# Kernel tuning notes

Hardware: AMD Instinct MI355X
Metric: run time of the kernel (lower is better)

Reference implementation:

```python
import jax, jax.numpy as jnp
import numpy as np

B, S, D = 2, 1024, 512
E, K = 8, 2          # num_experts, top_k (hardcoded in EncoderLayerMOE)
HMOE = 4             # SMoE_MHA heads
HD = D // HMOE       # 128 head dim for local experts
HID = 4 * D          # 2048 expert hidden (both extractors)
AH = 4               # attention heads
DK = D // AH
NEG = -1e9


def layer_norm(x, w, b, eps=1e-12):
    mu = x.mean(-1, keepdims=True)
    var = ((x - mu) ** 2).mean(-1, keepdims=True)
    return (x - mu) * jax.lax.rsqrt(var + eps) * w + b


def moe(x, gate_w, gate_b, w1, b1, w2, b2):
    """Dense all-expert SMoE, gather top-k, re-softmax topk weights (faithful).
    x: [..., d]; w1: [E,d,H]; w2: [E,H,d]."""
    gate_scores = x @ gate_w + gate_b                      # [..., E]
    sm = jax.nn.softmax(gate_scores, axis=-1)
    topk_s, topk_i = jax.lax.top_k(sm, K)                  # [..., K]
    h1 = jax.nn.relu(jnp.einsum('...d,edh->...eh', x, w1) + b1)   # [..., E, H]
    out = jnp.einsum('...eh,ehd->...ed', h1, w2) + b2      # [..., E, d]
    idx = jnp.broadcast_to(topk_i[..., None], topk_i.shape + (out.shape[-1],))
    sel = jnp.take_along_axis(out, idx, axis=-2)           # [..., K, d]
    w = jax.nn.softmax(topk_s, axis=-1)[..., None]         # re-softmax of topk scores
    return (sel * w).sum(-2)


def local_extractor(x, pre_w, pre_b, gate_w, gate_b, w1, b1, w2, b2, align_w, align_b):
    b, s, d = x.shape
    xp = x @ pre_w + pre_b
    xf = xp.reshape(b, s, HMOE, HD).transpose(0, 2, 1, 3)  # [b,h,s,hd]
    eo = moe(xf, gate_w, gate_b, w1, b1, w2, b2)
    xf = xf + eo
    xo = xf.transpose(0, 2, 1, 3).reshape(b, s, d)
    return xo @ align_w + align_b


def mha(xq, xkv, mask, wq, bq, wk, bk, wv, bv, wo, bo):
    b, sq, d = xq.shape
    sk = xkv.shape[1]
    q = (xq @ wq + bq).reshape(b, sq, AH, DK).transpose(0, 2, 1, 3)
    k = (xkv @ wk + bk).reshape(b, sk, AH, DK).transpose(0, 2, 1, 3)
    v = (xkv @ wv + bv).reshape(b, sk, AH, DK).transpose(0, 2, 1, 3)
    scores = jnp.einsum('bhqd,bhkd->bhqk', q, k) / jnp.sqrt(jnp.float32(DK))
    m = mask[:, None, :, :]                                 # [b,1,1,sk]
    scores = jnp.where(m, scores, NEG)
    attn = jax.nn.softmax(scores, axis=-1)
    attn = jnp.where(m, attn, 0.0)
    o = jnp.einsum('bhqk,bhkd->bhqd', attn, v)
    o = o.transpose(0, 2, 1, 3).reshape(b, sq, d)
    return o @ wo + bo


def setup_inputs() -> dict:
    key = jax.random.key(0)
    ks = iter(jax.random.split(key, 64))
    def p(shape, scale=0.02):
        return (jax.random.normal(next(ks), shape, jnp.float32) * scale)
    z = lambda *s: jnp.zeros(s, jnp.float32)
    o = lambda *s: jnp.ones(s, jnp.float32)
    return dict(
        x=jax.random.normal(next(ks), (B, S, D), jnp.float32),
        pre_w=p((D, D)), pre_b=z(D),
        l_gate_w=p((HD, E)), l_gate_b=z(E),
        l_w1=p((E, HD, HID)), l_b1=z(E, HID),
        l_w2=p((E, HID, HD)), l_b2=z(E, HD),
        align_w=p((D, D)), align_b=z(D),
        ln1_w=o(D), ln1_b=z(D),
        wq=p((D, D)), bq=z(D), wk=p((D, D)), bk=z(D),
        wv=p((D, D)), bv=z(D), wo=p((D, D)), bo=z(D),
        ln2_w=o(D), ln2_b=z(D),
        g_gate_w=p((D, E)), g_gate_b=z(E),
        g_w1=p((E, D, HID)), g_b1=z(E, HID),
        g_w2=p((E, HID, D)), g_b2=z(E, D),
        mask=jnp.ones((B, 1, S), bool),
    )


def reference(x, pre_w, pre_b, l_gate_w, l_gate_b, l_w1, l_b1, l_w2, l_b2,
              align_w, align_b, ln1_w, ln1_b, wq, bq, wk, bk, wv, bv, wo, bo,
              ln2_w, ln2_b, g_gate_w, g_gate_b, g_w1, g_b1, g_w2, g_b2, mask):
    # EncoderLayerMOE.forward, eval mode, normalize_before=True, cache=None
    residual = x
    xl = local_extractor(x, pre_w, pre_b, l_gate_w, l_gate_b,
                         l_w1, l_b1, l_w2, l_b2, align_w, align_b)
    xn = layer_norm(xl, ln1_w, ln1_b)
    att = mha(xn, xn, mask, wq, bq, wk, bk, wv, bv, wo, bo)
    x1 = residual + att
    residual = x1
    x2 = layer_norm(x1, ln2_w, ln2_b)
    g = moe(x2, g_gate_w, g_gate_b, g_w1, g_b1, g_w2, g_b2)
    out = residual + g
    return out
```

## Files before the change

kernel.cpp:

```cpp
#include <hip/hip_runtime.h>

typedef unsigned short ushort_t;
typedef __attribute__((ext_vector_type(8))) short short8;
typedef __attribute__((ext_vector_type(4))) short short4v;
typedef __attribute__((ext_vector_type(4))) float f32x4;

constexpr int B_    = 2;
constexpr int S_    = 1024;
constexpr int D_    = 512;
constexpr int E_    = 8;
constexpr int HMOE_ = 4;
constexpr int HD_   = 128;
constexpr int HID_  = 2048;
constexpr int AH_   = 4;
constexpr int NTOK  = B_ * S_;
constexpr int NSUB  = B_ * HMOE_ * S_;

#define DEVINL __device__ __forceinline__

DEVINL ushort_t f2bf(float f) {
    union { float f; unsigned int i; } c;
    c.f = f;
    unsigned int x = c.i;
    return (ushort_t)((x + 0x7fffu + ((x >> 16) & 1u)) >> 16);
}

template <bool ADD_R>
__global__ __launch_bounds__(256) void gemm_bias_k(
    const float* __restrict__ A, const float* __restrict__ W,
    const float* __restrict__ bias, const float* __restrict__ R,
    float* __restrict__ C, int M, int N, int Kd)
{
    __shared__ float As[16][68];
    __shared__ float Bs[16][68];
    const int tid = threadIdx.x;
    const int tx = tid & 15, ty = tid >> 4;
    const int m0 = blockIdx.y * 64, n0 = blockIdx.x * 64;
    float acc[4][4] = {};
    for (int k0 = 0; k0 < Kd; k0 += 16) {
        #pragma unroll
        for (int j = 0; j < 4; j++) {
            int i = tid + 256 * j;
            int mm = i >> 4, kk = i & 15;
            As[kk][mm] = A[(size_t)(m0 + mm) * Kd + k0 + kk];
        }
        {
            int row = tid >> 4, col = (tid & 15) * 4;
            float4 bv = *reinterpret_cast<const float4*>(W + (size_t)(k0 + row) * N + n0 + col);
            *reinterpret_cast<float4*>(&Bs[row][col]) = bv;
        }
        __syncthreads();
        #pragma unroll
        for (int kk = 0; kk < 16; kk++) {
            float4 a = *reinterpret_cast<const float4*>(&As[kk][ty * 4]);
            float4 b = *reinterpret_cast<const float4*>(&Bs[kk][tx * 4]);
            float av[4] = {a.x, a.y, a.z, a.w};
            float bv[4] = {b.x, b.y, b.z, b.w};
            #pragma unroll
            for (int i = 0; i < 4; i++)
                #pragma unroll
                for (int j = 0; j < 4; j++)
                    acc[i][j] = fmaf(av[i], bv[j], acc[i][j]);
        }
        __syncthreads();
    }
    #pragma unroll
    for (int i = 0; i < 4; i++) {
        int m = m0 + ty * 4 + i;
        #pragma unroll
        for (int j = 0; j < 4; j++) {
            int n = n0 + tx * 4 + j;
            float v = acc[i][j] + bias[n];
            if (ADD_R) v += R[(size_t)m * N + n];
            C[(size_t)m * N + n] = v;
        }
    }
}

template <bool OUTF, bool OUTBF, bool ADD_R>
__global__ __launch_bounds__(256) void gemm_mfma_k(
    const ushort_t* __restrict__ A, const ushort_t* __restrict__ WT,
    const float* __restrict__ bias, const float* __restrict__ R,
    float* __restrict__ C, ushort_t* __restrict__ Cbf)
{
    __shared__ ushort_t As[64 * 72];
    __shared__ ushort_t Bs[64 * 72];
    const int tid = threadIdx.x;
    const int lane = tid & 63, wv = tid >> 6;
    const int l15 = lane & 15, l4 = lane >> 4;
    const int m0 = blockIdx.y * 64, n0 = blockIdx.x * 64;

    f32x4 acc[4];
    #pragma unroll
    for (int mi = 0; mi < 4; mi++) acc[mi] = (f32x4){0.f, 0.f, 0.f, 0.f};

    const int sr = tid >> 2, ss = (tid & 3) * 16;
    for (int k0 = 0; k0 < 512; k0 += 64) {
        __syncthreads();
        {
            const ushort_t* ap = A + (size_t)(m0 + sr) * 512 + k0 + ss;
            ushort_t* dst = &As[sr * 72 + ss];
            *reinterpret_cast<short8*>(dst)     = *reinterpret_cast<const short8*>(ap);
            *reinterpret_cast<short8*>(dst + 8) = *reinterpret_cast<const short8*>(ap + 8);
            const ushort_t* wp = WT + (size_t)(n0 + sr) * 512 + k0 + ss;
            ushort_t* dstb = &Bs[sr * 72 + ss];
            *reinterpret_cast<short8*>(dstb)     = *reinterpret_cast<const short8*>(wp);
            *reinterpret_cast<short8*>(dstb + 8) = *reinterpret_cast<const short8*>(wp + 8);
        }
        __syncthreads();
        #pragma unroll
        for (int ks = 0; ks < 2; ks++) {
            short8 bfr = *reinterpret_cast<const short8*>(&Bs[(wv * 16 + l15) * 72 + ks * 32 + l4 * 8]);
            #pragma unroll
            for (int mi = 0; mi < 4; mi++) {
                short8 af = *reinterpret_cast<const short8*>(&As[(mi * 16 + l15) * 72 + ks * 32 + l4 * 8]);
                acc[mi] = __builtin_amdgcn_mfma_f32_16x16x32_bf16(af, bfr, acc[mi], 0, 0, 0);
            }
        }
    }
    const int n = n0 + wv * 16 + l15;
    float bv = bias[n];
    #pragma unroll
    for (int mi = 0; mi < 4; mi++) {
        #pragma unroll
        for (int r = 0; r < 4; r++) {
            int m = m0 + mi * 16 + l4 * 4 + r;
            float v = acc[mi][r] + bv;
            if (ADD_R) v += R[(size_t)m * 512 + n];
            if (OUTF)  C[(size_t)m * 512 + n] = v;
            if (OUTBF) Cbf[(size_t)m * 512 + n] = f2bf(v);
        }
    }
}

template <bool OUTF, bool EMIT_BF>
__global__ __launch_bounds__(256) void ln_k(
    const float* __restrict__ X, const float* __restrict__ w,
    const float* __restrict__ b, float* __restrict__ Y, ushort_t* __restrict__ Ybf)
{
    __shared__ float red[8];
    const int row = blockIdx.x, tid = threadIdx.x;
    const float* x = X + (size_t)row * D_;
    float v0 = x[tid], v1 = x[tid + 256];
    float s = v0 + v1, ss = v0 * v0 + v1 * v1;
    #pragma unroll
    for (int off = 32; off; off >>= 1) {
        s  += __shfl_xor(s, off);
        ss += __shfl_xor(ss, off);
    }
    if ((tid & 63) == 0) { red[tid >> 6] = s; red[(tid >> 6) + 4] = ss; }
    __syncthreads();
    float mu  = (red[0] + red[1] + red[2] + red[3]) * (1.f / D_);
    float var = (red[4] + red[5] + red[6] + red[7]) * (1.f / D_) - mu * mu;
    float rs = rsqrtf(var + 1e-12f);
    float y0 = (v0 - mu) * rs * w[tid]       + b[tid];
    float y1 = (v1 - mu) * rs * w[tid + 256] + b[tid + 256];
    if (OUTF) {
        Y[(size_t)row * D_ + tid]       = y0;
        Y[(size_t)row * D_ + tid + 256] = y1;
    }
    if (EMIT_BF) {
        Ybf[(size_t)row * D_ + tid]       = f2bf(y0);
        Ybf[(size_t)row * D_ + tid + 256] = f2bf(y1);
    }
}

DEVINL size_t local_off(int t) {
    int bq = t >> 12, r = t & 4095, h = r >> 10, sI = r & 1023;
    return ((size_t)(bq * S_ + sI)) * D_ + (size_t)h * HD_;
}

__global__ __launch_bounds__(256) void wconv_k(
    const float* __restrict__ in, ushort_t* __restrict__ out, int R, int C)
{
    __shared__ float tile[64][65];
    const int e = blockIdx.z;
    const int c0 = blockIdx.x * 64, r0 = blockIdx.y * 64;
    const float* src = in + ((size_t)e * R + r0) * C + c0;
    const int cl = threadIdx.x & 63, rl = threadIdx.x >> 6;
    #pragma unroll
    for (int j = 0; j < 16; j++) {
        int rr = rl * 16 + j;
        tile[rr][cl] = src[(size_t)rr * C + cl];
    }
    __syncthreads();
    ushort_t* dst = out + ((size_t)e * C + c0) * R + r0;
    #pragma unroll
    for (int j = 0; j < 16; j++) {
        int cc = rl * 16 + j;
        dst[(size_t)cc * R + cl] = f2bf(tile[cl][cc]);
    }
}

__global__ __launch_bounds__(256) void f2bf_k(
    const float* __restrict__ X, ushort_t* __restrict__ Y, int n)
{
    int i = (blockIdx.x * 256 + threadIdx.x) * 4;
    if (i < n) {
        float4 v = *reinterpret_cast<const float4*>(X + i);
        short4v o;
        o.x = (short)f2bf(v.x); o.y = (short)f2bf(v.y);
        o.z = (short)f2bf(v.z); o.w = (short)f2bf(v.w);
        *reinterpret_cast<short4v*>(Y + i) = o;
    }
}

__global__ __launch_bounds__(256) void vtrans_bf_k(
    const ushort_t* __restrict__ Vbf, ushort_t* __restrict__ VT)
{
    __shared__ ushort_t tile[64][68];
    const int s0 = blockIdx.x * 64;
    const int d0 = blockIdx.y * 64;
    const int bh = blockIdx.z;
    const int b = bh >> 2, h = bh & 3;
    const ushort_t* src = Vbf + (size_t)(b * S_ + s0) * D_ + h * HD_ + d0;
    const int cl = threadIdx.x & 63, rl = threadIdx.x >> 6;
    #pragma unroll
    for (int j = 0; j < 16; j++) {
        int rr = rl * 16 + j;
        tile[rr][cl] = src[(size_t)rr * D_ + cl];
    }
    __syncthreads();
    ushort_t* dst = VT + ((size_t)bh * HD_ + d0) * S_ + s0;
    #pragma unroll
    for (int j = 0; j < 16; j++) {
        int cc = rl * 16 + j;
        dst[(size_t)cc * S_ + cl] = tile[cl][cc];
    }
}

template <bool LOCAL>
__global__ __launch_bounds__(256) void gate_score_k(
    const float* __restrict__ X, const float* __restrict__ gwm,
    const float* __restrict__ gb, int2* __restrict__ choice,
    float2* __restrict__ cweight)
{
    constexpr int DIMD = LOCAL ? HD_ : D_;
    constexpr int PL = DIMD / 64;
    const int t = blockIdx.x * 4 + (threadIdx.x >> 6);
    const int lane = threadIdx.x & 63;
    const float* x = X + (LOCAL ? local_off(t) : (size_t)t * D_);
    float xr[PL];
    #pragma unroll
    for (int i = 0; i < PL; i++) xr[i] = x[lane + 64 * i];
    float sc[8];
    #pragma unroll
    for (int e = 0; e < 8; e++) {
        float a = 0.f;
        #pragma unroll
        for (int i = 0; i < PL; i++)
            a = fmaf(xr[i], gwm[(size_t)(lane + 64 * i) * E_ + e], a);
        #pragma unroll
        for (int o2 = 32; o2; o2 >>= 1) a += __shfl_xor(a, o2);
        sc[e] = a;
    }
    if (lane == 0) {
        float mx = -1e30f;
        #pragma unroll
        for (int e = 0; e < 8; e++) { sc[e] += gb[e]; mx = fmaxf(mx, sc[e]); }
        float p[8], psum = 0.f;
        #pragma unroll
        for (int e = 0; e < 8; e++) { p[e] = expf(sc[e] - mx); psum += p[e]; }
        float inv = 1.f / psum;
        #pragma unroll
        for (int e = 0; e < 8; e++) p[e] *= inv;
        int i0 = 0;
        for (int e = 1; e < 8; e++) if (p[e] > p[i0]) i0 = e;
        int i1 = (i0 == 0) ? 1 : 0;
        for (int e = 0; e < 8; e++) if (e != i0 && p[e] > p[i1]) i1 = e;
        float e0 = expf(p[i0]), e1 = expf(p[i1]);
        float wnorm = 1.f / (e0 + e1);
        choice[t]  = (int2){i0, i1};
        cweight[t] = (float2){e0 * wnorm, e1 * wnorm};
    }
}

template <int CAP>
__global__ __launch_bounds__(256) void gate_build_k(
    const int2* __restrict__ choice, const float2* __restrict__ cweight,
    int* __restrict__ cnt, int* __restrict__ idx, float* __restrict__ gwv)
{
    __shared__ int wtot[4];
    __shared__ int basesh;
    const int e = blockIdx.x;
    const int tid = threadIdx.x;
    const int lane = tid & 63, wv = tid >> 6;
    if (tid == 0) basesh = 0;
    __syncthreads();
    for (int t0 = 0; t0 < CAP; t0 += 256) {
        int t = t0 + tid;
        int2 ch = choice[t];
        float2 cw = cweight[t];
        bool m0 = (ch.x == e);
        bool m = m0 | (ch.y == e);
        float w = m0 ? cw.x : cw.y;
        unsigned long long mask = __ballot(m);
        int posw = __popcll(mask & ((1ull << lane) - 1ull));
        if (lane == 0) wtot[wv] = __popcll(mask);
        __syncthreads();
        int base = basesh;
        int woff = 0, tot = 0;
        #pragma unroll
        for (int i = 0; i < 4; i++) {
            int c = wtot[i];
            tot += c;
            if (i < wv) woff += c;
        }
        if (m) {
            int p = base + woff + posw;
            idx[e * CAP + p] = t;
            gwv[e * CAP + p] = w;
        }
        __syncthreads();
        if (tid == 0) basesh = base + tot;
    }
    __syncthreads();
    int total = basesh;
    if (tid == 0) cnt[e] = total;
    int padEnd = (total + 63) & ~63;
    if (padEnd > CAP) padEnd = CAP;
    for (int p = total + tid; p < padEnd; p += 256) {
        idx[e * CAP + p] = 0;
        gwv[e * CAP + p] = 0.f;
    }
}

__global__ void prefix_k(const int* __restrict__ cnt, int* __restrict__ prefix)
{
    if (threadIdx.x == 0) {
        int s = 0;
        for (int e = 0; e < 8; e++) { prefix[e] = s; s += cnt[e]; }
    }
}

template <int DIMD, int GSPLIT>
__global__ __launch_bounds__(256, 3) void ffn_grouped3_k(
    const ushort_t* __restrict__ Xbf,
    const ushort_t* __restrict__ w1t, const float* __restrict__ b1,
    const ushort_t* __restrict__ w2t, const float* __restrict__ b2,
    const int* __restrict__ cnt, const int* __restrict__ idx,
    const float* __restrict__ gwv, float* __restrict__ OUT)
{
    constexpr int K1  = DIMD;
    constexpr int NT2 = DIMD / 128;
    constexpr int CAP = (DIMD == HD_) ? NSUB : NTOK;
    constexpr int HC  = 128;
    constexpr int CHUNKS = HID_ / HC / GSPLIT;
    constexpr bool PIPE = (NT2 == 1);

    __shared__ ushort_t bufA[64 * 72];
    __shared__ ushort_t bufB[128 * 72];
    __shared__ ushort_t Hs[64 * 136];
    __shared__ float    gws[64];
    __shared__ size_t   toffs[64];

    const int tid  = threadIdx.x;
    const int lane = tid & 63;
    const int wv   = tid >> 6;
    const int e    = blockIdx.x & 7;
    const int rest = blockIdx.x >> 3;
    const int mt   = rest / GSPLIT;
    const int g    = rest % GSPLIT;
    const int m0   = mt * 64;

    if (m0 >= cnt[e]) return;

    if (tid < 64) {
        int t = idx[e * CAP + m0 + tid];
        toffs[tid] = (DIMD == HD_) ? local_off(t) : (size_t)t * D_;
        gws[tid]   = gwv[e * CAP + m0 + tid];
    }
    __syncthreads();

    const int l15 = lane & 15, l4 = lane >> 4;
    const int ar = tid >> 2, as = (tid & 3) * 16;
    const int bn = tid >> 1, bs = (tid & 1) * 32;

    f32x4 accO[NT2][4][2];
    #pragma unroll
    for (int n2 = 0; n2 < NT2; n2++)
        #pragma unroll
        for (int mi = 0; mi < 4; mi++)
            #pragma unroll
            for (int ni = 0; ni < 2; ni++)
                accO[n2][mi][ni] = (f32x4){0.f, 0.f, 0.f, 0.f};

    const ushort_t* w1e = w1t + (size_t)e * HID_ * K1;
    const ushort_t* w2e = w2t + (size_t)e * DIMD * HID_;
    const float* b1e = b1 + (size_t)e * HID_;

    short8 ra0, ra1, rb0, rb1, rb2, rb3;

    const int hc0 = g * CHUNKS * HC;
    for (int hc = hc0; hc < hc0 + CHUNKS * HC; hc += HC) {
        f32x4 acc1[4][2];
        #pragma unroll
        for (int mi = 0; mi < 4; mi++)
            #pragma unroll
            for (int ni = 0; ni < 2; ni++)
                acc1[mi][ni] = (f32x4){0.f, 0.f, 0.f, 0.f};

        if (PIPE) {
            const ushort_t* xp = Xbf + toffs[ar] + as;
            ra0 = *reinterpret_cast<const short8*>(xp);
            ra1 = *reinterpret_cast<const short8*>(xp + 8);
            const ushort_t* wp = w1e + (size_t)(hc + bn) * K1 + bs;
            rb0 = *reinterpret_cast<const short8*>(wp);
            rb1 = *reinterpret_cast<const short8*>(wp + 8);
            rb2 = *reinterpret_cast<const short8*>(wp + 16);
            rb3 = *reinterpret_cast<const short8*>(wp + 24);
        }

        for (int k0 = 0; k0 < K1; k0 += 64) {
            __syncthreads();
// ... 63 lines not shown
        #pragma unroll
        for (int mi = 0; mi < 4; mi++)
            #pragma unroll
            for (int ni = 0; ni < 2; ni++) {
                float bb = (ni == 0) ? b1v0 : b1v1;
                #pragma unroll
                for (int r = 0; r < 4; r++) {
                    int row = mi * 16 + l4 * 4 + r;
                    int col = wv * 32 + ni * 16 + l15;
                    Hs[row * 136 + col] = f2bf(fmaxf(acc1[mi][ni][r] + bb, 0.f));
                }
            }

        #pragma unroll
        for (int n2 = 0; n2 < NT2; n2++) {
            #pragma unroll
            for (int k2t = 0; k2t < 2; k2t++) {
                __syncthreads();
                if (PIPE) {
                    ushort_t* dst = &bufB[bn * 72 + bs];
                    *reinterpret_cast<short8*>(dst)      = rb0;
                    *reinterpret_cast<short8*>(dst + 8)  = rb1;
                    *reinterpret_cast<short8*>(dst + 16) = rb2;
                    *reinterpret_cast<short8*>(dst + 24) = rb3;
                    if (!(n2 == NT2 - 1 && k2t == 1)) {
                        int nn2 = (k2t == 1) ? n2 + 1 : n2;
                        int nk  = (k2t == 1) ? 0 : 1;
                        const ushort_t* wp = w2e + (size_t)(nn2 * 128 + bn) * HID_ + hc + nk * 64 + bs;
                        rb0 = *reinterpret_cast<const short8*>(wp);
                        rb1 = *reinterpret_cast<const short8*>(wp + 8);
                        rb2 = *reinterpret_cast<const short8*>(wp + 16);
                        rb3 = *reinterpret_cast<const short8*>(wp + 24);
                    }
                } else {
                    const ushort_t* wp = w2e + (size_t)(n2 * 128 + bn) * HID_ + hc + k2t * 64 + bs;
                    ushort_t* dst = &bufB[bn * 72 + bs];
                    #pragma unroll
                    for (int j = 0; j < 32; j += 8)
                        *reinterpret_cast<short8*>(dst + j) = *reinterpret_cast<const short8*>(wp + j);
                }
                __syncthreads();
                #pragma unroll
                for (int ks = 0; ks < 2; ks++) {
                    short8 af[4], bfr[2];
                    #pragma unroll
                    for (int mi = 0; mi < 4; mi++)
                        af[mi] = *reinterpret_cast<const short8*>(&Hs[(mi * 16 + l15) * 136 + k2t * 64 + ks * 32 + l4 * 8]);
                    #pragma unroll
                    for (int ni = 0; ni < 2; ni++)
                        bfr[ni] = *reinterpret_cast<const short8*>(&bufB[(wv * 32 + ni * 16 + l15) * 72 + ks * 32 + l4 * 8]);
                    #pragma unroll
                    for (int mi = 0; mi < 4; mi++)
                        #pragma unroll
                        for (int ni = 0; ni < 2; ni++)
                            accO[n2][mi][ni] = __builtin_amdgcn_mfma_f32_16x16x32_bf16(
                                af[mi], bfr[ni], accO[n2][mi][ni], 0, 0, 0);
                }
            }
        }
    }

    #pragma unroll
    for (int n2 = 0; n2 < NT2; n2++) {
        float b2v0 = (g == 0) ? b2[(size_t)e * DIMD + n2 * 128 + wv * 32 + l15] : 0.f;
        float b2v1 = (g == 0) ? b2[(size_t)e * DIMD + n2 * 128 + wv * 32 + 16 + l15] : 0.f;
        #pragma unroll
        for (int mi = 0; mi < 4; mi++)
            #pragma unroll
            for (int r = 0; r < 4; r++) {
                int row = mi * 16 + l4 * 4 + r;
                float gg = gws[row];
                if (gg != 0.f) {
                    float* op = OUT + toffs[row] + n2 * 128 + wv * 32;
                    atomicAdd(op + l15,      gg * (accO[n2][mi][0][r] + b2v0));
                    atomicAdd(op + 16 + l15, gg * (accO[n2][mi][1][r] + b2v1));
                }
            }
    }
}

__global__ __launch_bounds__(256) void ffn1g_k(
    const ushort_t* __restrict__ Xbf,
    const ushort_t* __restrict__ w1t, const float* __restrict__ b1,
    const int* __restrict__ cnt, const int* __restrict__ prefix,
    const int* __restrict__ idx, int hbase, ushort_t* __restrict__ Hbuf)
{
    __shared__ ushort_t bufA[64 * 72];
    __shared__ ushort_t bufB[128 * 72];
    __shared__ size_t   toffs[64];
    __shared__ int      sbase;

    const int tid  = threadIdx.x;
    const int lane = tid & 63;
    const int wv   = tid >> 6;
    const int e    = blockIdx.x & 7;
    const int rest = blockIdx.x >> 3;
    const int mt   = rest >> 3;
    const int hs   = rest & 7;
    const int m0   = mt * 64;
    const int ce   = cnt[e];
    if (m0 >= ce) return;

    if (tid < 64) toffs[tid] = (size_t)idx[e * NTOK + m0 + tid] * D_;
    if (tid == 0) sbase = prefix[e];
    __syncthreads();

    const int l15 = lane & 15, l4 = lane >> 4;
    const int ar = tid >> 2, as = (tid & 3) * 16;
    const int bn = tid >> 1, bs = (tid & 1) * 32;
    const int hc = hbase + hs * 128;

    const ushort_t* w1e = w1t + (size_t)e * HID_ * D_;

    f32x4 acc1[4][2];
    #pragma unroll
    for (int mi = 0; mi < 4; mi++)
        #pragma unroll
        for (int ni = 0; ni < 2; ni++)
            acc1[mi][ni] = (f32x4){0.f, 0.f, 0.f, 0.f};

    short8 ra0, ra1, rb0, rb1, rb2, rb3;
    {
        const ushort_t* xp = Xbf + toffs[ar] + as;
        ra0 = *reinterpret_cast<const short8*>(xp);
        ra1 = *reinterpret_cast<const short8*>(xp + 8);
        const ushort_t* wp = w1e + (size_t)(hc + bn) * D_ + bs;
        rb0 = *reinterpret_cast<const short8*>(wp);
        rb1 = *reinterpret_cast<const short8*>(wp + 8);
        rb2 = *reinterpret_cast<const short8*>(wp + 16);
        rb3 = *reinterpret_cast<const short8*>(wp + 24);
    }
    for (int k0 = 0; k0 < D_; k0 += 64) {
        __syncthreads();
        {
            ushort_t* dst = &bufA[ar * 72 + as];
            *reinterpret_cast<short8*>(dst)     = ra0;
            *reinterpret_cast<short8*>(dst + 8) = ra1;
            ushort_t* dstb = &bufB[bn * 72 + bs];
            *reinterpret_cast<short8*>(dstb)      = rb0;
            *reinterpret_cast<short8*>(dstb + 8)  = rb1;
            *reinterpret_cast<short8*>(dstb + 16) = rb2;
            *reinterpret_cast<short8*>(dstb + 24) = rb3;
        }
        if (k0 + 64 < D_) {
            const ushort_t* xp = Xbf + toffs[ar] + k0 + 64 + as;
            ra0 = *reinterpret_cast<const short8*>(xp);
            ra1 = *reinterpret_cast<const short8*>(xp + 8);
            const ushort_t* wp = w1e + (size_t)(hc + bn) * D_ + k0 + 64 + bs;
            rb0 = *reinterpret_cast<const short8*>(wp);
            rb1 = *reinterpret_cast<const short8*>(wp + 8);
            rb2 = *reinterpret_cast<const short8*>(wp + 16);
            rb3 = *reinterpret_cast<const short8*>(wp + 24);
        }
        __syncthreads();
        #pragma unroll
        for (int ks = 0; ks < 2; ks++) {
            short8 af[4], bfr[2];
            #pragma unroll
            for (int mi = 0; mi < 4; mi++)
                af[mi] = *reinterpret_cast<const short8*>(&bufA[(mi * 16 + l15) * 72 + ks * 32 + l4 * 8]);
            #pragma unroll
            for (int ni = 0; ni < 2; ni++)
                bfr[ni] = *reinterpret_cast<const short8*>(&bufB[(wv * 32 + ni * 16 + l15) * 72 + ks * 32 + l4 * 8]);
            #pragma unroll
            for (int mi = 0; mi < 4; mi++)
                #pragma unroll
                for (int ni = 0; ni < 2; ni++)
                    acc1[mi][ni] = __builtin_amdgcn_mfma_f32_16x16x32_bf16(
                        af[mi], bfr[ni], acc1[mi][ni], 0, 0, 0);
        }
    }

    const int slotbase = sbase + m0;
    const int hout = (hc - hbase);
    float b1v0 = b1[(size_t)e * HID_ + hc + wv * 32 + l15];
    float b1v1 = b1[(size_t)e * HID_ + hc + wv * 32 + 16 + l15];
    #pragma unroll
    for (int mi = 0; mi < 4; mi++)
        #pragma unroll
        for (int ni = 0; ni < 2; ni++) {
            float bb = (ni == 0) ? b1v0 : b1v1;
            #pragma unroll
            for (int r = 0; r < 4; r++) {
                int row = mi * 16 + l4 * 4 + r;
                if (m0 + row < ce) {
                    int col = hout + wv * 32 + ni * 16 + l15;
                    Hbuf[(size_t)(slotbase + row) * 1024 + col] =
                        f2bf(fmaxf(acc1[mi][ni][r] + bb, 0.f));
                }
            }
        }
}

template <bool ADD_B2>
__global__ __launch_bounds__(256) void ffn2g_k(
    const ushort_t* __restrict__ Hbuf,
    const ushort_t* __restrict__ w2t, const float* __restrict__ b2,
    const int* __restrict__ cnt, const int* __restrict__ prefix,
    const int* __restrict__ idx, const float* __restrict__ gwv,
    int hbase, float* __restrict__ OUT)
{
    __shared__ ushort_t bufA[32 * 72];
    __shared__ ushort_t bufB[128 * 72];
    __shared__ float    gws[32];
    __shared__ size_t   toffs[32];
    __shared__ int      sbase;

    const int tid  = threadIdx.x;
    const int lane = tid & 63;
    const int wv   = tid >> 6;
    const int e    = blockIdx.x & 7;
    const int rest = blockIdx.x >> 3;
    const int mt   = rest >> 2;
    const int n2   = rest & 3;
    const int m0   = mt * 32;
    const int ce   = cnt[e];
    if (m0 >= ce) return;

    if (tid < 32) {
        toffs[tid] = (size_t)idx[e * NTOK + m0 + tid] * D_;
        gws[tid]   = gwv[e * NTOK + m0 + tid];
    }
    if (tid == 0) sbase = prefix[e];
    __syncthreads();

    const int l15 = lane & 15, l4 = lane >> 4;
    const int ar = tid >> 3, as = (tid & 7) * 8;
    const int bn = tid >> 1, bs = (tid & 1) * 32;
    const int slot0 = sbase + m0;

    const ushort_t* w2e = w2t + (size_t)e * D_ * HID_;
    const ushort_t* Hb  = Hbuf + (size_t)slot0 * 1024;

    f32x4 acc[2][2];
    #pragma unroll
    for (int mi = 0; mi < 2; mi++)
        #pragma unroll
        for (int ni = 0; ni < 2; ni++)
            acc[mi][ni] = (f32x4){0.f, 0.f, 0.f, 0.f};

    short8 ra0, rb0, rb1, rb2, rb3;
    {
        ra0 = *reinterpret_cast<const short8*>(Hb + (size_t)ar * 1024 + as);
        const ushort_t* wp = w2e + (size_t)(n2 * 128 + bn) * HID_ + hbase + bs;
        rb0 = *reinterpret_cast<const short8*>(wp);
        rb1 = *reinterpret_cast<const short8*>(wp + 8);
        rb2 = *reinterpret_cast<const short8*>(wp + 16);
        rb3 = *reinterpret_cast<const short8*>(wp + 24);
    }
    for (int k0 = 0; k0 < 1024; k0 += 64) {
        __syncthreads();
        {
            *reinterpret_cast<short8*>(&bufA[ar * 72 + as]) = ra0;
            ushort_t* dstb = &bufB[bn * 72 + bs];
            *reinterpret_cast<short8*>(dstb)      = rb0;
            *reinterpret_cast<short8*>(dstb + 8)  = rb1;
            *reinterpret_cast<short8*>(dstb + 16) = rb2;
            *reinterpret_cast<short8*>(dstb + 24) = rb3;
        }
        if (k0 + 64 < 1024) {
            ra0 = *reinterpret_cast<const short8*>(Hb + (size_t)ar * 1024 + k0 + 64 + as);
            const ushort_t* wp = w2e + (size_t)(n2 * 128 + bn) * HID_ + hbase + k0 + 64 + bs;
            rb0 = *reinterpret_cast<const short8*>(wp);
            rb1 = *reinterpret_cast<const short8*>(wp + 8);
            rb2 = *reinterpret_cast<const short8*>(wp + 16);
            rb3 = *reinterpret_cast<const short8*>(wp + 24);
        }
        __syncthreads();
        #pragma unroll
        for (int ks = 0; ks < 2; ks++) {
            short8 af[2], bfr[2];
            #pragma unroll
            for (int mi = 0; mi < 2; mi++)
                af[mi] = *reinterpret_cast<const short8*>(&bufA[(mi * 16 + l15) * 72 + ks * 32 + l4 * 8]);
            #pragma unroll
            for (int ni = 0; ni < 2; ni++)
                bfr[ni] = *reinterpret_cast<const short8*>(&bufB[(wv * 32 + ni * 16 + l15) * 72 + ks * 32 + l4 * 8]);
            #pragma unroll
            for (int mi = 0; mi < 2; mi++)
                #pragma unroll
                for (int ni = 0; ni < 2; ni++)
                    acc[mi][ni] = __builtin_amdgcn_mfma_f32_16x16x32_bf16(
                        af[mi], bfr[ni], acc[mi][ni], 0, 0, 0);
        }
    }

    float b2v0 = ADD_B2 ? b2[(size_t)e * D_ + n2 * 128 + wv * 32 + l15] : 0.f;
    float b2v1 = ADD_B2 ? b2[(size_t)e * D_ + n2 * 128 + wv * 32 + 16 + l15] : 0.f;
    #pragma unroll
    for (int mi = 0; mi < 2; mi++)
        #pragma unroll
        for (int r = 0; r < 4; r++) {
            int row = mi * 16 + l4 * 4 + r;
            float g = gws[row];
            if (g != 0.f) {
                float* op = OUT + toffs[row] + n2 * 128 + wv * 32;
                atomicAdd(op + l15,      g * (acc[mi][0][r] + b2v0));
                atomicAdd(op + 16 + l15, g * (acc[mi][1][r] + b2v1));
            }
        }
}

template <int DIMD>
__global__ __launch_bounds__(256) void ffn_grouped_k(
    const float* __restrict__ Xf,
    const float* __restrict__ w1f, const float* __restrict__ b1,
// ... 408 lines not shown
                    o[i2][0] = fmaf(pa[i2], vv.x, o[i2][0]);
                    o[i2][1] = fmaf(pa[i2], vv.y, o[i2][1]);
                    o[i2][2] = fmaf(pa[i2], vv.z, o[i2][2]);
                    o[i2][3] = fmaf(pa[i2], vv.w, o[i2][3]);
                }
            }
        }
        __syncthreads();
    }

    #pragma unroll
    for (int i2 = 0; i2 < 4; i2++) {
        float inv = 1.f / lrow[py * 4 + i2];
        float4 ov;
        ov.x = o[i2][0] * inv; ov.y = o[i2][1] * inv;
        ov.z = o[i2][2] * inv; ov.w = o[i2][3] * inv;
        *reinterpret_cast<float4*>(AO + base + (size_t)(q0 + py * 4 + i2) * D_ + px * 4) = ov;
    }
}

__global__ __launch_bounds__(256) void copy_out_k(
    const float* __restrict__ X, float* __restrict__ Y, int n)
{
    int base = (blockIdx.x * 256 + threadIdx.x) * 4;
    if (base < n)
        *reinterpret_cast<float4*>(Y + base) = *reinterpret_cast<const float4*>(X + base);
}

extern "C" void kernel_launch(void* const* d_in, const int* in_sizes, int n_in,
                              void* d_out, int out_size, void* d_ws, size_t ws_size,
                              hipStream_t stream)
{
    (void)in_sizes; (void)n_in; (void)out_size;
    const float* x        = (const float*)d_in[0];
    const float* pre_w    = (const float*)d_in[1];
    const float* pre_b    = (const float*)d_in[2];
    const float* l_gate_w = (const float*)d_in[3];
    const float* l_gate_b = (const float*)d_in[4];
    const float* l_w1     = (const float*)d_in[5];
    const float* l_b1     = (const float*)d_in[6];
    const float* l_w2     = (const float*)d_in[7];
    const float* l_b2     = (const float*)d_in[8];
    const float* align_w  = (const float*)d_in[9];
    const float* align_b  = (const float*)d_in[10];
    const float* ln1_w    = (const float*)d_in[11];
    const float* ln1_b    = (const float*)d_in[12];
    const float* wq       = (const float*)d_in[13];
    const float* bq       = (const float*)d_in[14];
    const float* wk       = (const float*)d_in[15];
    const float* bk       = (const float*)d_in[16];
    const float* wv       = (const float*)d_in[17];
    const float* bv       = (const float*)d_in[18];
    const float* wo       = (const float*)d_in[19];
    const float* bo       = (const float*)d_in[20];
    const float* ln2_w    = (const float*)d_in[21];
    const float* ln2_b    = (const float*)d_in[22];
    const float* g_gate_w = (const float*)d_in[23];
    const float* g_gate_b = (const float*)d_in[24];
    const float* g_w1     = (const float*)d_in[25];
    const float* g_b1     = (const float*)d_in[26];
    const float* g_w2     = (const float*)d_in[27];
    const float* g_b2     = (const float*)d_in[28];

    char* ws = (char*)d_ws;
    const size_t MB  = 1024 * 1024;
    const size_t MB4 = (size_t)NTOK * D_ * sizeof(float);
    float* W0 = (float*)(ws + 0 * MB);
    float* W1 = (float*)(ws + 4 * MB);
    float* W2 = (float*)(ws + 8 * MB);

    const bool pre = ws_size >= (size_t)59 * MB;

    char* blob = ws + (pre ? 12 : 16) * MB;
    int*    cntl = (int*)(blob);
    int*    cntg = (int*)(blob + 32);
    int*    idxl = (int*)(blob + 64);
    int*    idxg = (int*)(blob + 64 + 262144);
    float*  gwvl = (float*)(blob + 64 + 262144 + 65536);
    float*  gwvg = (float*)(blob + 64 + 262144 + 65536 + 262144);
    int2*   chl  = (int2*)(blob + 64 + 262144 + 65536 + 262144 + 65536);
    float2* cwl  = (float2*)((char*)chl + 65536);
    int2*   chg  = (int2*)((char*)cwl + 65536);
    float2* cwg  = (float2*)((char*)chg + 16384);
    int*    prefg = (int*)((char*)cwg + 16384);

    ushort_t* x_bf = (ushort_t*)(ws + 12 * MB);
    ushort_t* preT   = (ushort_t*)(ws + 14 * MB);
    ushort_t* alignT = (ushort_t*)(ws + 14 * MB + 512 * 1024);
    ushort_t* wqT    = (ushort_t*)(ws + 15 * MB);
    ushort_t* wkT    = (ushort_t*)(ws + 15 * MB + 512 * 1024);
    ushort_t* wvT    = (ushort_t*)(ws + 16 * MB);
    ushort_t* woT    = (ushort_t*)(ws + 16 * MB + 512 * 1024);
    ushort_t* XBF  = (ushort_t*)(ws + 17 * MB);
    ushort_t* Vbf  = (ushort_t*)(ws + 4 * MB);
    ushort_t* VTb  = (ushort_t*)(ws + 6 * MB);
    ushort_t* Qbf  = (ushort_t*)(ws + 8 * MB);
    ushort_t* Kbf  = (ushort_t*)(ws + 10 * MB);
    ushort_t* Hbuf = (ushort_t*)(ws + 4 * MB);
    ushort_t* LW1T = (ushort_t*)(ws + 19 * MB);
    ushort_t* LW2T = (ushort_t*)(ws + 23 * MB);
    ushort_t* GW1T = (ushort_t*)(ws + 27 * MB);
    ushort_t* GW2T = (ushort_t*)(ws + 43 * MB);
    float* W3 = (float*)(ws + 12 * MB);

    const dim3 gg(D_ / 64, NTOK / 64);

    if (pre) {
        f2bf_k<<<(NTOK * D_) / (256 * 4), 256, 0, stream>>>(x, x_bf, NTOK * D_);
        wconv_k<<<dim3(8, 8, 1), 256, 0, stream>>>(pre_w,   preT,   D_, D_);
        wconv_k<<<dim3(8, 8, 1), 256, 0, stream>>>(align_w, alignT, D_, D_);
        wconv_k<<<dim3(8, 8, 1), 256, 0, stream>>>(wq, wqT, D_, D_);
        wconv_k<<<dim3(8, 8, 1), 256, 0, stream>>>(wk, wkT, D_, D_);
        wconv_k<<<dim3(8, 8, 1), 256, 0, stream>>>(wv, wvT, D_, D_);
        wconv_k<<<dim3(8, 8, 1), 256, 0, stream>>>(wo, woT, D_, D_);
        wconv_k<<<dim3(HID_ / 64, HD_ / 64, 8),  256, 0, stream>>>(l_w1, LW1T, HD_,  HID_);
        wconv_k<<<dim3(HD_ / 64,  HID_ / 64, 8), 256, 0, stream>>>(l_w2, LW2T, HID_, HD_);
        wconv_k<<<dim3(HID_ / 64, D_ / 64, 8),   256, 0, stream>>>(g_w1, GW1T, D_,   HID_);
        wconv_k<<<dim3(D_ / 64,   HID_ / 64, 8), 256, 0, stream>>>(g_w2, GW2T, HID_, D_);

        gemm_mfma_k<true, true, false><<<gg, 256, 0, stream>>>(x_bf, preT, pre_b, nullptr, W0, XBF);
        gate_score_k<true><<<NSUB / 4, 256, 0, stream>>>(W0, l_gate_w, l_gate_b, chl, cwl);
        gate_build_k<NSUB><<<8, 256, 0, stream>>>(chl, cwl, cntl, idxl, gwvl);
        hipMemcpyAsync(W1, W0, MB4, hipMemcpyDeviceToDevice, stream);
        ffn_grouped3_k<HD_, 4><<<8 * (NSUB / 64) * 4, 256, 0, stream>>>(
            XBF, LW1T, l_b1, LW2T, l_b2, cntl, idxl, gwvl, W1);
        f2bf_k<<<(NTOK * D_) / (256 * 4), 256, 0, stream>>>(W1, XBF, NTOK * D_);
        gemm_mfma_k<true, false, false><<<gg, 256, 0, stream>>>(XBF, alignT, align_b, nullptr, W2, nullptr);
        ln_k<false, true><<<NTOK, 256, 0, stream>>>(W2, ln1_w, ln1_b, W0, XBF);
        gemm_mfma_k<false, true, false><<<gg, 256, 0, stream>>>(XBF, wqT, bq, nullptr, nullptr, Qbf);
        gemm_mfma_k<false, true, false><<<gg, 256, 0, stream>>>(XBF, wkT, bk, nullptr, nullptr, Kbf);
        gemm_mfma_k<false, true, false><<<gg, 256, 0, stream>>>(XBF, wvT, bv, nullptr, nullptr, Vbf);
        vtrans_bf_k<<<dim3(16, 2, 8), 256, 0, stream>>>(Vbf, VTb);
        fattn_mfma_k<<<dim3(S_ / 32, B_ * AH_), 256, 0, stream>>>(Qbf, Kbf, VTb, XBF);
        gemm_mfma_k<true, false, true><<<gg, 256, 0, stream>>>(XBF, woT, bo, x, W0, nullptr);
        ln_k<true, true><<<NTOK, 256, 0, stream>>>(W0, ln2_w, ln2_b, W2, XBF);
        gate_score_k<false><<<NTOK / 4, 256, 0, stream>>>(W2, g_gate_w, g_gate_b, chg, cwg);
        gate_build_k<NTOK><<<8, 256, 0, stream>>>(chg, cwg, cntg, idxg, gwvg);
        prefix_k<<<1, 64, 0, stream>>>(cntg, prefg);
        ffn1g_k<<<8 * 32 * 8, 256, 0, stream>>>(
            XBF, GW1T, g_b1, cntg, prefg, idxg, 0, Hbuf);
        ffn2g_k<true><<<8 * 64 * 4, 256, 0, stream>>>(
            Hbuf, GW2T, g_b2, cntg, prefg, idxg, gwvg, 0, W0);
        ffn1g_k<<<8 * 32 * 8, 256, 0, stream>>>(
            XBF, GW1T, g_b1, cntg, prefg, idxg, 1024, Hbuf);
        ffn2g_k<false><<<8 * 64 * 4, 256, 0, stream>>>(
            Hbuf, GW2T, g_b2, cntg, prefg, idxg, gwvg, 1024, W0);
        copy_out_k<<<(NTOK * D_) / (256 * 4), 256, 0, stream>>>(W0, (float*)d_out, NTOK * D_);
    } else {
        gemm_bias_k<false><<<gg, 256, 0, stream>>>(x, pre_w, pre_b, nullptr, W0, NTOK, D_, D_);
        gate_score_k<true><<<NSUB / 4, 256, 0, stream>>>(W0, l_gate_w, l_gate_b, chl, cwl);
        gate_build_k<NSUB><<<8, 256, 0, stream>>>(chl, cwl, cntl, idxl, gwvl);
        hipMemcpyAsync(W1, W0, MB4, hipMemcpyDeviceToDevice, stream);
        ffn_grouped_k<HD_><<<8 * (NSUB / 64), 256, 0, stream>>>(
            W0, l_w1, l_b1, l_w2, l_b2, cntl, idxl, gwvl, W1);
        gemm_bias_k<false><<<gg, 256, 0, stream>>>(W1, align_w, align_b, nullptr, W2, NTOK, D_, D_);
        ln_k<true, false><<<NTOK, 256, 0, stream>>>(W2, ln1_w, ln1_b, W0, nullptr);
        gemm_bias_k<false><<<gg, 256, 0, stream>>>(W0, wq, bq, nullptr, W1, NTOK, D_, D_);
        gemm_bias_k<false><<<gg, 256, 0, stream>>>(W0, wk, bk, nullptr, W2, NTOK, D_, D_);
        gemm_bias_k<false><<<gg, 256, 0, stream>>>(W0, wv, bv, nullptr, W3, NTOK, D_, D_);
        fattn_k<<<dim3(S_ / QT, B_ * AH_), 256, 0, stream>>>(W1, W2, W3, W1);
        gemm_bias_k<true><<<gg, 256, 0, stream>>>(W1, wo, bo, x, W0, NTOK, D_, D_);
        ln_k<true, false><<<NTOK, 256, 0, stream>>>(W0, ln2_w, ln2_b, W2, nullptr);
        gate_score_k<false><<<NTOK / 4, 256, 0, stream>>>(W2, g_gate_w, g_gate_b, chg, cwg);
        gate_build_k<NTOK><<<8, 256, 0, stream>>>(chg, cwg, cntg, idxg, gwvg);
        ffn_grouped_k<D_><<<8 * (NTOK / 64) * 4, 256, 0, stream>>>(
            W2, g_w1, g_b1, g_w2, g_b2, cntg, idxg, gwvg, W0);
        copy_out_k<<<(NTOK * D_) / (256 * 4), 256, 0, stream>>>(W0, (float*)d_out, NTOK * D_);
    }
}
```

Measured before the change: 468.6 us.

## Fuse QKV projections, weight conversions and MoE residual, and drop extra passes

The three Q/K/V projection GEMMs become one launch that picks its weight and bias by block index. The six square weight transposes are batched into one launch. The local MoE now accumulates directly into the pre-projection output instead of a copied buffer, removing a device-to-device memcpy. The align GEMM converts fp32 activations to bf16 during its shared-memory load, replacing a separate f2bf pass, and the one-thread prefix kernel is replaced by per-block prefix sums of the expert counts. This cuts launch count and global memory round trips, at the cost of redundant fp32 loads and conversion inside the GEMM tile loop.

```diff
diff --git a/kernel.cpp b/kernel.cpp
--- a/kernel.cpp
+++ b/kernel.cpp
@@ -77,9 +77,10 @@
     }
 }
 
-template <bool OUTF, bool OUTBF, bool ADD_R>
+template <bool INF32, bool OUTF, bool OUTBF, bool ADD_R>
 __global__ __launch_bounds__(256) void gemm_mfma_k(
-    const ushort_t* __restrict__ A, const ushort_t* __restrict__ WT,
+    const ushort_t* __restrict__ A, const float* __restrict__ Af,
+    const ushort_t* __restrict__ WT,
     const float* __restrict__ bias, const float* __restrict__ R,
     float* __restrict__ C, ushort_t* __restrict__ Cbf)
 {
@@ -89,6 +90,77 @@
     const int lane = tid & 63, wv = tid >> 6;
     const int l15 = lane & 15, l4 = lane >> 4;
     const int m0 = blockIdx.y * 64, n0 = blockIdx.x * 64;
+
+    f32x4 acc[4];
+    #pragma unroll
+    for (int mi = 0; mi < 4; mi++) acc[mi] = (f32x4){0.f, 0.f, 0.f, 0.f};
+
+    const int sr = tid >> 2, ss = (tid & 3) * 16;
+    for (int k0 = 0; k0 < 512; k0 += 64) {
+        __syncthreads();
+        if (INF32) {
+            const float* ap = Af + (size_t)(m0 + sr) * 512 + k0 + ss;
+            ushort_t* dst = &As[sr * 72 + ss];
+            #pragma unroll
+            for (int j = 0; j < 16; j += 4) {
+                float4 v = *reinterpret_cast<const float4*>(ap + j);
+                dst[j + 0] = f2bf(v.x); dst[j + 1] = f2bf(v.y);
+                dst[j + 2] = f2bf(v.z); dst[j + 3] = f2bf(v.w);
+            }
+        } else {
+            const ushort_t* ap = A + (size_t)(m0 + sr) * 512 + k0 + ss;
+            ushort_t* dst = &As[sr * 72 + ss];
+            *reinterpret_cast<short8*>(dst)     = *reinterpret_cast<const short8*>(ap);
+            *reinterpret_cast<short8*>(dst + 8) = *reinterpret_cast<const short8*>(ap + 8);
+        }
+        {
+            const ushort_t* wp = WT + (size_t)(n0 + sr) * 512 + k0 + ss;
+            ushort_t* dstb = &Bs[sr * 72 + ss];
+            *reinterpret_cast<short8*>(dstb)     = *reinterpret_cast<const short8*>(wp);
+            *reinterpret_cast<short8*>(dstb + 8) = *reinterpret_cast<const short8*>(wp + 8);
+        }
+        __syncthreads();
+        #pragma unroll
+        for (int ks = 0; ks < 2; ks++) {
+            short8 bfr = *reinterpret_cast<const short8*>(&Bs[(wv * 16 + l15) * 72 + ks * 32 + l4 * 8]);
+            #pragma unroll
+            for (int mi = 0; mi < 4; mi++) {
+                short8 af = *reinterpret_cast<const short8*>(&As[(mi * 16 + l15) * 72 + ks * 32 + l4 * 8]);
+                acc[mi] = __builtin_amdgcn_mfma_f32_16x16x32_bf16(af, bfr, acc[mi], 0, 0, 0);
+            }
+        }
+    }
+    const int n = n0 + wv * 16 + l15;
+    float bv = bias[n];
+    #pragma unroll
+    for (int mi = 0; mi < 4; mi++) {
+        #pragma unroll
+        for (int r = 0; r < 4; r++) {
+            int m = m0 + mi * 16 + l4 * 4 + r;
+            float v = acc[mi][r] + bv;
+            if (ADD_R) v += R[(size_t)m * 512 + n];
+            if (OUTF)  C[(size_t)m * 512 + n] = v;
+            if (OUTBF) Cbf[(size_t)m * 512 + n] = f2bf(v);
+        }
+    }
+}
+
+struct QKVW { const ushort_t* wt[3]; const float* bias[3]; ushort_t* out[3]; };
+
+__global__ __launch_bounds__(256) void gemm_qkv_k(
+    const ushort_t* __restrict__ A, QKVW p)
+{
+    __shared__ ushort_t As[64 * 72];
+    __shared__ ushort_t Bs[64 * 72];
+    const int tid = threadIdx.x;
+    const int lane = tid & 63, wv = tid >> 6;
+    const int l15 = lane & 15, l4 = lane >> 4;
+    const int sel = blockIdx.x >> 3;
+    const int n0 = (blockIdx.x & 7) * 64;
+    const int m0 = blockIdx.y * 64;
+    const ushort_t* WT = p.wt[sel];
+    const float* bias = p.bias[sel];
+    ushort_t* Cbf = p.out[sel];
 
     f32x4 acc[4];
     #pragma unroll
@@ -125,10 +197,7 @@
         #pragma unroll
         for (int r = 0; r < 4; r++) {
             int m = m0 + mi * 16 + l4 * 4 + r;
-            float v = acc[mi][r] + bv;
-            if (ADD_R) v += R[(size_t)m * 512 + n];
-            if (OUTF)  C[(size_t)m * 512 + n] = v;
-            if (OUTBF) Cbf[(size_t)m * 512 + n] = f2bf(v);
+            Cbf[(size_t)m * 512 + n] = f2bf(acc[mi][r] + bv);
         }
     }
 }
@@ -189,6 +258,30 @@
     for (int j = 0; j < 16; j++) {
         int cc = rl * 16 + j;
         dst[(size_t)cc * R + cl] = f2bf(tile[cl][cc]);
+    }
+}
+
+struct WC6 { const float* src[6]; ushort_t* dst[6]; };
+__global__ __launch_bounds__(256) void wconv6_k(WC6 a)
+{
+    __shared__ float tile[64][65];
+    const int w = blockIdx.z;
+    const float* in = a.src[w];
+    ushort_t* out = a.dst[w];
+    const int c0 = blockIdx.x * 64, r0 = blockIdx.y * 64;
+    const float* src = in + (size_t)r0 * D_ + c0;
+    const int cl = threadIdx.x & 63, rl = threadIdx.x >> 6;
+    #pragma unroll
+    for (int j = 0; j < 16; j++) {
+        int rr = rl * 16 + j;
+        tile[rr][cl] = src[(size_t)rr * D_ + cl];
+    }
+    __syncthreads();
+    ushort_t* dst = out + (size_t)c0 * D_ + r0;
+    #pragma unroll
+    for (int j = 0; j < 16; j++) {
+        int cc = rl * 16 + j;
+        dst[(size_t)cc * D_ + cl] = f2bf(tile[cl][cc]);
     }
 }
 
@@ -322,14 +415,6 @@
     for (int p = total + tid; p < padEnd; p += 256) {
         idx[e * CAP + p] = 0;
         gwv[e * CAP + p] = 0.f;
-    }
-}
-
-__global__ void prefix_k(const int* __restrict__ cnt, int* __restrict__ prefix)
-{
-    if (threadIdx.x == 0) {
-        int s = 0;
-        for (int e = 0; e < 8; e++) { prefix[e] = s; s += cnt[e]; }
     }
 }
 
@@ -559,8 +644,8 @@
 __global__ __launch_bounds__(256) void ffn1g_k(
     const ushort_t* __restrict__ Xbf,
     const ushort_t* __restrict__ w1t, const float* __restrict__ b1,
-    const int* __restrict__ cnt, const int* __restrict__ prefix,
-    const int* __restrict__ idx, int hbase, ushort_t* __restrict__ Hbuf)
+    const int* __restrict__ cnt, const int* __restrict__ idx,
+    int hbase, ushort_t* __restrict__ Hbuf)
 {
     __shared__ ushort_t bufA[64 * 72];
     __shared__ ushort_t bufB[128 * 72];
@@ -579,7 +664,11 @@
     if (m0 >= ce) return;
 
     if (tid < 64) toffs[tid] = (size_t)idx[e * NTOK + m0 + tid] * D_;
-    if (tid == 0) sbase = prefix[e];
+    if (tid == 0) {
+        int s = 0;
+        for (int j = 0; j < e; j++) s += cnt[j];
+        sbase = s;
+    }
     __syncthreads();
 
     const int l15 = lane & 15, l4 = lane >> 4;
@@ -673,9 +762,8 @@
 __global__ __launch_bounds__(256) void ffn2g_k(
     const ushort_t* __restrict__ Hbuf,
     const ushort_t* __restrict__ w2t, const float* __restrict__ b2,
-    const int* __restrict__ cnt, const int* __restrict__ prefix,
-    const int* __restrict__ idx, const float* __restrict__ gwv,
-    int hbase, float* __restrict__ OUT)
+    const int* __restrict__ cnt, const int* __restrict__ idx,
+    const float* __restrict__ gwv, int hbase, float* __restrict__ OUT)
 {
     __shared__ ushort_t bufA[32 * 72];
     __shared__ ushort_t bufB[128 * 72];
@@ -698,7 +786,11 @@
         toffs[tid] = (size_t)idx[e * NTOK + m0 + tid] * D_;
         gws[tid]   = gwv[e * NTOK + m0 + tid];
     }
-    if (tid == 0) sbase = prefix[e];
+    if (tid == 0) {
+        int s = 0;
+        for (int j = 0; j < e; j++) s += cnt[j];
+        sbase = s;
+    }
     __syncthreads();
 
     const int l15 = lane & 15, l4 = lane >> 4;
@@ -1273,7 +1365,6 @@
     float2* cwl  = (float2*)((char*)chl + 65536);
     int2*   chg  = (int2*)((char*)cwl + 65536);
     float2* cwg  = (float2*)((char*)chg + 16384);
-    int*    prefg = (int*)((char*)cwg + 16384);
 
     ushort_t* x_bf = (ushort_t*)(ws + 12 * MB);
     ushort_t* preT   = (ushort_t*)(ws + 14 * MB);
@@ -1298,44 +1389,50 @@
 
     if (pre) {
         f2bf_k<<<(NTOK * D_) / (256 * 4), 256, 0, stream>>>(x, x_bf, NTOK * D_);
-        wconv_k<<<dim3(8, 8, 1), 256, 0, stream>>>(pre_w,   preT,   D_, D_);
-        wconv_k<<<dim3(8, 8, 1), 256, 0, stream>>>(align_w, alignT, D_, D_);
-        wconv_k<<<dim3(8, 8, 1), 256, 0, stream>>>(wq, wqT, D_, D_);
-        wconv_k<<<dim3(8, 8, 1), 256, 0, stream>>>(wk, wkT, D_, D_);
-        wconv_k<<<dim3(8, 8, 1), 256, 0, stream>>>(wv, wvT, D_, D_);
-        wconv_k<<<dim3(8, 8, 1), 256, 0, stream>>>(wo, woT, D_, D_);
+        {
+            WC6 wc;
+            wc.src[0] = pre_w; wc.src[1] = align_w; wc.src[2] = wq;
+            wc.src[3] = wk;    wc.src[4] = wv;      wc.src[5] = wo;
+            wc.dst[0] = preT;  wc.dst[1] = alignT;  wc.dst[2] = wqT;
+            wc.dst[3] = wkT;   wc.dst[4] = wvT;     wc.dst[5] = woT;
+            wconv6_k<<<dim3(8, 8, 6), 256, 0, stream>>>(wc);
+        }
         wconv_k<<<dim3(HID_ / 64, HD_ / 64, 8),  256, 0, stream>>>(l_w1, LW1T, HD_,  HID_);
         wconv_k<<<dim3(HD_ / 64,  HID_ / 64, 8), 256, 0, stream>>>(l_w2, LW2T, HID_, HD_);
         wconv_k<<<dim3(HID_ / 64, D_ / 64, 8),   256, 0, stream>>>(g_w1, GW1T, D_,   HID_);
         wconv_k<<<dim3(D_ / 64,   HID_ / 64, 8), 256, 0, stream>>>(g_w2, GW2T, HID_, D_);
 
-        gemm_mfma_k<true, true, false><<<gg, 256, 0, stream>>>(x_bf, preT, pre_b, nullptr, W0, XBF);
+        gemm_mfma_k<false, true, true, false><<<gg, 256, 0, stream>>>(
+            x_bf, nullptr, preT, pre_b, nullptr, W0, XBF);
         gate_score_k<true><<<NSUB / 4, 256, 0, stream>>>(W0, l_gate_w, l_gate_b, chl, cwl);
         gate_build_k<NSUB><<<8, 256, 0, stream>>>(chl, cwl, cntl, idxl, gwvl);
-        hipMemcpyAsync(W1, W0, MB4, hipMemcpyDeviceToDevice, stream);
         ffn_grouped3_k<HD_, 4><<<8 * (NSUB / 64) * 4, 256, 0, stream>>>(
-            XBF, LW1T, l_b1, LW2T, l_b2, cntl, idxl, gwvl, W1);
-        f2bf_k<<<(NTOK * D_) / (256 * 4), 256, 0, stream>>>(W1, XBF, NTOK * D_);
-        gemm_mfma_k<true, false, false><<<gg, 256, 0, stream>>>(XBF, alignT, align_b, nullptr, W2, nullptr);
+            XBF, LW1T, l_b1, LW2T, l_b2, cntl, idxl, gwvl, W0);
+        gemm_mfma_k<true, true, false, false><<<gg, 256, 0, stream>>>(
+            nullptr, W0, alignT, align_b, nullptr, W2, nullptr);
         ln_k<false, true><<<NTOK, 256, 0, stream>>>(W2, ln1_w, ln1_b, W0, XBF);
-        gemm_mfma_k<false, true, false><<<gg, 256, 0, stream>>>(XBF, wqT, bq, nullptr, nullptr, Qbf);
-        gemm_mfma_k<false, true, false><<<gg, 256, 0, stream>>>(XBF, wkT, bk, nullptr, nullptr, Kbf);
-        gemm_mfma_k<false, true, false><<<gg, 256, 0, stream>>>(XBF, wvT, bv, nullptr, nullptr, Vbf);
+        {
+            QKVW qp;
+            qp.wt[0] = wqT; qp.wt[1] = wkT; qp.wt[2] = wvT;
+            qp.bias[0] = bq; qp.bias[1] = bk; qp.bias[2] = bv;
+            qp.out[0] = Qbf; qp.out[1] = Kbf; qp.out[2] = Vbf;
+            gemm_qkv_k<<<dim3(24, 32), 256, 0, stream>>>(XBF, qp);
+        }
         vtrans_bf_k<<<dim3(16, 2, 8), 256, 0, stream>>>(Vbf, VTb);
         fattn_mfma_k<<<dim3(S_ / 32, B_ * AH_), 256, 0, stream>>>(Qbf, Kbf, VTb, XBF);
-        gemm_mfma_k<true, false, true><<<gg, 256, 0, stream>>>(XBF, woT, bo, x, W0, nullptr);
+        gemm_mfma_k<false, true, false, true><<<gg, 256, 0, stream>>>(
+            XBF, nullptr, woT, bo, x, W0, nullptr);
         ln_k<true, true><<<NTOK, 256, 0, stream>>>(W0, ln2_w, ln2_b, W2, XBF);
         gate_score_k<false><<<NTOK / 4, 256, 0, stream>>>(W2, g_gate_w, g_gate_b, chg, cwg);
         gate_build_k<NTOK><<<8, 256, 0, stream>>>(chg, cwg, cntg, idxg, gwvg);
-        prefix_k<<<1, 64, 0, stream>>>(cntg, prefg);
         ffn1g_k<<<8 * 32 * 8, 256, 0, stream>>>(
-            XBF, GW1T, g_b1, cntg, prefg, idxg, 0, Hbuf);
+            XBF, GW1T, g_b1, cntg, idxg, 0, Hbuf);
         ffn2g_k<true><<<8 * 64 * 4, 256, 0, stream>>>(
-            Hbuf, GW2T, g_b2, cntg, prefg, idxg, gwvg, 0, W0);
+            Hbuf, GW2T, g_b2, cntg, idxg, gwvg, 0, W0);
         ffn1g_k<<<8 * 32 * 8, 256, 0, stream>>>(
-            XBF, GW1T, g_b1, cntg, prefg, idxg, 1024, Hbuf);
+            XBF, GW1T, g_b1, cntg, idxg, 1024, Hbuf);
         ffn2g_k<false><<<8 * 64 * 4, 256, 0, stream>>>(
-            Hbuf, GW2T, g_b2, cntg, prefg, idxg, gwvg, 1024, W0);
+            Hbuf, GW2T, g_b2, cntg, idxg, gwvg, 1024, W0);
         copy_out_k<<<(NTOK * D_) / (256 * 4), 256, 0, stream>>>(W0, (float*)d_out, NTOK * D_);
     } else {
         gemm_bias_k<false><<<gg, 256, 0, stream>>>(x, pre_w, pre_b, nullptr, W0, NTOK, D_, D_);
```

New measurement: 439.8 us. -6.1%, faster.
